# Optimization experiments

Measured on AMD Instinct MI355X. Metric: run time of the kernel, lower is better.

## Reference

```python
import jax, jax.numpy as jnp
import numpy as np

TEMP = 0.0005

def conv1d(x, w, b):
    # x: [B, Cin, T], w: [Cout, Cin, K] -> [B, Cout, T] with SAME padding
    out = jax.lax.conv_general_dilated(x, w, (1,), 'SAME', dimension_numbers=('NCH', 'OIH', 'NCH'))
    return out + b[None, :, None]

def setup_inputs() -> dict:
    key = jax.random.key(0)
    ks = jax.random.split(key, 24)
    B, Cs, T1 = 16, 80, 1000   # spec channels / mel frames
    Ct, T2 = 512, 200          # text channels / phonemes
    Ca, G = 80, 256            # attention channels / speaker embedding
    n = lambda i, shape: jax.random.normal(ks[i], shape, jnp.float32)
    w = lambda i, shape: n(i, shape) * 0.05
    return {
        'queries': n(0, (B, Cs, T1)),
        'keys': n(1, (B, Ct, T2)),
        'mask': jnp.ones((B, T2), jnp.int32),
        'attn_prior': jax.random.uniform(ks[2], (B, T1, T2), jnp.float32),
        'g': n(3, (B, G)),
        # key_proj: Conv(Ct -> 2Ct, k=3) -> ReLU -> Conv(2Ct -> Ca, k=1)
        'wk1': w(4, (2 * Ct, Ct, 3)), 'bk1': jnp.zeros((2 * Ct,), jnp.float32),
        'wk2': w(5, (Ca, 2 * Ct, 1)), 'bk2': jnp.zeros((Ca,), jnp.float32),
        # query_proj: Conv(Cs -> 2Cs, k=3) -> ReLU -> Conv(2Cs -> Cs, k=1) -> ReLU -> Conv(Cs -> Ca, k=1)
        'wq1': w(6, (2 * Cs, Cs, 3)), 'bq1': jnp.zeros((2 * Cs,), jnp.float32),
        'wq2': w(7, (Cs, 2 * Cs, 1)), 'bq2': jnp.zeros((Cs,), jnp.float32),
        'wq3': w(8, (Ca, Cs, 1)), 'bq3': jnp.zeros((Ca,), jnp.float32),
        # speaker projections (LinearNorm): gin -> n_text_channels / n_spec_channels
        'w_kspk': w(9, (Ct, G)), 'b_kspk': jnp.zeros((Ct,), jnp.float32),
        'w_qspk': w(10, (Cs, G)), 'b_qspk': jnp.zeros((Cs,), jnp.float32),
    }

def reference(queries, keys, mask, attn_prior, g, wk1, bk1, wk2, bk2, wq1, bq1, wq2, bq2, wq3, bq3, w_kspk, b_kspk, w_qspk, b_qspk):
    # speaker conditioning: same projected vector added at every time step
    keys = keys + (g @ w_kspk.T + b_kspk)[:, :, None]
    queries = queries + (g @ w_qspk.T + b_qspk)[:, :, None]
    # projections
    k_enc = conv1d(jax.nn.relu(conv1d(keys, wk1, bk1)), wk2, bk2)              # [B, Ca, T2]
    q = jax.nn.relu(conv1d(queries, wq1, bq1))
    q = jax.nn.relu(conv1d(q, wq2, bq2))
    q_enc = conv1d(q, wq3, bq3)                                                # [B, Ca, T1]
    # squared L2 distance via GEMM trick: |q|^2 + |k|^2 - 2 q.k  (same math as broadcast diff)
    q2 = jnp.sum(q_enc * q_enc, axis=1)[:, :, None]                            # [B, T1, 1]
    k2 = jnp.sum(k_enc * k_enc, axis=1)[:, None, :]                            # [B, 1, T2]
    qk = jnp.einsum('bct,bcs->bts', q_enc, k_enc)                              # [B, T1, T2]
    attn = (-TEMP * (q2 + k2 - 2.0 * qk))[:, None]                             # [B, 1, T1, T2]
    attn = jax.nn.log_softmax(attn, axis=3) + jnp.log(attn_prior[:, None] + 1e-8)
    attn_logprob = attn
    neg_inf = jnp.where(mask[:, None, None, :] == 0, -jnp.inf, 0.0)
    attn = jax.nn.softmax(attn + neg_inf, axis=3)
    return attn, attn_logprob
```

## Files before the change

### kernel.cpp

```cpp
#include <hip/hip_runtime.h>
#include <hip/hip_bf16.h>
#include <math.h>

#define NB 16
#define CS 80
#define T1 1000
#define CT 512
#define T2 200
#define CA 80
#define GD 256
#define C2T 1024
#define C2S 160
#define TEMP_F 0.0005f
#define ENC_STR 96

typedef __attribute__((ext_vector_type(8))) short short8;
typedef __attribute__((ext_vector_type(4))) float floatx4;

__device__ __forceinline__ short f2bf(float x) {
    unsigned u = __builtin_bit_cast(unsigned, x);
    unsigned r = (u + 0x7fffu + ((u >> 16) & 1u)) >> 16;
    return (short)r;
}

template <int COUT, int CIN, int KW, int COP, int CINP>
__device__ __forceinline__ void wpack_body(const float* __restrict__ w,
                                           short* __restrict__ wp, int bid) {
    constexpr int NC32 = CINP / 32;
    constexpr int NFRAG = (COP / 16) * KW * NC32;
    int gid = bid * 256 + threadIdx.x;
    int frag = gid >> 6, lane = gid & 63;
    if (frag >= NFRAG) return;
    int co16 = frag / (KW * NC32), rem = frag - co16 * (KW * NC32);
    int k = rem / NC32, ci32 = rem - k * NC32;
    int co = co16 * 16 + (lane & 15);
    int ci = ci32 * 32 + (lane >> 4) * 8;
    short8 v;
#pragma unroll
    for (int j = 0; j < 8; j++) {
        float f = 0.f;
        if (co < COUT && ci + j < CIN) f = w[((size_t)co * CIN + ci + j) * KW + k];
        v[j] = f2bf(f);
    }
    *(short8*)(wp + (size_t)frag * 512 + lane * 8) = v;
}

template <int C, int T>
__device__ __forceinline__ void addspkT_body(const float* __restrict__ in,
                                             const float* __restrict__ g,
                                             const float* __restrict__ w_spk,
                                             const float* __restrict__ b_spk,
                                             short* __restrict__ outT,
                                             float* sm, int bx, int by, int b) {
    float* spkS = sm;
    float* S = sm + 32;
    const int t0 = bx * 64, c0 = by * 32;
    const int tid = threadIdx.x;
    int cl = tid >> 3, part = tid & 7;
    int c = c0 + cl;
    float s = 0.f;
    if (c < C) {
        const float* wr = w_spk + (size_t)c * GD;
        const float* gr = g + b * GD;
        int j0 = part * 32;
#pragma unroll
        for (int j = 0; j < 32; j++) s += gr[j0 + j] * wr[j0 + j];
    }
    s += __shfl_xor(s, 1, 64); s += __shfl_xor(s, 2, 64); s += __shfl_xor(s, 4, 64);
    if (part == 0) spkS[cl] = s + ((c < C) ? b_spk[c] : 0.f);
    __syncthreads();
    for (int i = tid; i < 32 * 64; i += 256) {
        int cll = i >> 6, tl = i & 63;
        int gc = c0 + cll, gt = t0 + tl;
        float v = 0.f;
        if (gc < C && gt < T) v = in[((size_t)b * C + gc) * T + gt] + spkS[cll];
        S[cll * 65 + tl] = v;
    }
    __syncthreads();
    for (int i = tid; i < 64 * 32; i += 256) {
        int tl = i >> 5, cll = i & 31;
        int gt = t0 + tl, gc = c0 + cll;
        if (gc < C && gt < T) outT[((size_t)b * T + gt) * C + gc] = f2bf(S[cll * 65 + tl]);
    }
}

__global__ __launch_bounds__(256) void prep_kernel(
    const float* __restrict__ keys, const float* __restrict__ queries, const float* __restrict__ g,
    const float* __restrict__ wk1, const float* __restrict__ wq1, const float* __restrict__ wk2,
    const float* __restrict__ wq2, const float* __restrict__ wq3,
    const float* __restrict__ w_kspk, const float* __restrict__ b_kspk,
    const float* __restrict__ w_qspk, const float* __restrict__ b_qspk,
    short* __restrict__ wk1p, short* __restrict__ wq1p, short* __restrict__ wk2p,
    short* __restrict__ wq2p, short* __restrict__ wq3p,
    short* __restrict__ xkT, short* __restrict__ xqT) {
    __shared__ float sm[32 + 32 * 65];
    int bid = blockIdx.x;
    if (bid < 768) { wpack_body<C2T, CT, 3, C2T, CT>(wk1, wk1p, bid); return; }
    bid -= 768;
    if (bid < 27) { wpack_body<C2S, CS, 3, 192, 96>(wq1, wq1p, bid); return; }
    bid -= 27;
    if (bid < 40) { wpack_body<CA, C2T, 1, 80, 1024>(wk2, wk2p, bid); return; }
    bid -= 40;
    if (bid < 7) { wpack_body<CA, C2S, 1, 80, 160>(wq2, wq2p, bid); return; }
    bid -= 7;
    if (bid < 4) { wpack_body<CA, CS, 1, 80, 96>(wq3, wq3p, bid); return; }
    bid -= 4;
    if (bid < 1024) {
        int bx = bid & 3, by = (bid >> 2) & 15, b = bid >> 6;
        addspkT_body<CT, T2>(keys, g, w_kspk, b_kspk, xkT, sm, bx, by, b);
        return;
    }
    bid -= 1024;
    {
        int bx = bid & 15, by = (bid >> 4) % 3, b = bid / 48;
        addspkT_body<CS, T1>(queries, g, w_qspk, b_qspk, xqT, sm, bx, by, b);
    }
}

template <int CIN, int COUT, int T, int KW, bool RELU, int CICH, int NC32T>
__device__ __forceinline__ void conv_body(const short* __restrict__ xT,
                                          const short* __restrict__ wp,
                                          const float* __restrict__ bias,
                                          short* __restrict__ outT,
                                          short* Xs, int bx, int by, int b) {
    constexpr int TT = 128, COT = 64;
    constexpr int PAD = KW / 2;
    constexpr int XROWS = TT + KW - 1;
    constexpr int PITCH = CICH + 8;
    constexpr int NPC = CICH / 8;
    constexpr int NC32 = CICH / 32;
    constexpr int CINP = NC32T * 32;
    constexpr int NCHK = CINP / CICH;
    constexpr int NPIECE = XROWS * NPC;
    constexpr int NLD = (NPIECE + 255) / 256;

    const int t0 = bx * TT, co0 = by * COT;
    const int tid = threadIdx.x, wave = tid >> 6, lane = tid & 63;
    const int quad = lane >> 4, l16 = lane & 15;
    const int wt = wave * 32;
    const int co16_0 = co0 >> 4;
    const short* xb = xT + (size_t)b * T * CIN;

    floatx4 acc[4][2];
#pragma unroll
    for (int mi = 0; mi < 4; mi++)
#pragma unroll
        for (int ni = 0; ni < 2; ni++) acc[mi][ni] = (floatx4){0.f, 0.f, 0.f, 0.f};

    for (int i = tid; i < NPIECE; i += 256) {
        int r = i / NPC, p = i - r * NPC;
        int t = t0 + r - PAD, ci = p * 8;
        uint4 v = {0u, 0u, 0u, 0u};
        if ((unsigned)t < (unsigned)T && ci + 8 <= CIN)
            v = *(const uint4*)(xb + (size_t)t * CIN + ci);
        *(uint4*)(Xs + r * PITCH + p * 8) = v;
    }
    __syncthreads();

    for (int kc = 0; kc < NCHK; kc++) {
        uint4 tmp[NLD];
        if (NCHK > 1 && kc + 1 < NCHK) {
            int ci0n = (kc + 1) * CICH;
#pragma unroll
            for (int ld = 0; ld < NLD; ld++) {
                int i = tid + ld * 256;
                tmp[ld] = (uint4){0u, 0u, 0u, 0u};
                if (i < NPIECE) {
                    int r = i / NPC, p = i - r * NPC;
                    int t = t0 + r - PAD, ci = ci0n + p * 8;
                    if ((unsigned)t < (unsigned)T && ci + 8 <= CIN)
                        tmp[ld] = *(const uint4*)(xb + (size_t)t * CIN + ci);
                }
            }
        }
        const short* Xb = Xs + (NCHK > 1 ? (kc & 1) : 0) * XROWS * PITCH;
#pragma unroll
        for (int k = 0; k < KW; k++) {
#pragma unroll
            for (int kk = 0; kk < NC32; kk++) {
                int ci32 = kc * NC32 + kk;
                short8 a[4];
#pragma unroll
                for (int mi = 0; mi < 4; mi++)
                    a[mi] = *(const short8*)(wp +
                        ((size_t)((co16_0 + mi) * KW + k) * NC32T + ci32) * 512 + lane * 8);
#pragma unroll
                for (int ni = 0; ni < 2; ni++) {
                    short8 bb = *(const short8*)(Xb + (wt + ni * 16 + l16 + k) * PITCH +
                                                 kk * 32 + quad * 8);
#pragma unroll
                    for (int mi = 0; mi < 4; mi++)
                        acc[mi][ni] = __builtin_amdgcn_mfma_f32_16x16x32_bf16(a[mi], bb,
                                                                              acc[mi][ni], 0, 0, 0);
                }
            }
        }
        if (NCHK > 1 && kc + 1 < NCHK) {
            short* Xn = Xs + ((kc + 1) & 1) * XROWS * PITCH;
#pragma unroll
            for (int ld = 0; ld < NLD; ld++) {
                int i = tid + ld * 256;
                if (i < NPIECE) {
                    int r = i / NPC, p = i - r * NPC;
                    *(uint4*)(Xn + r * PITCH + p * 8) = tmp[ld];
                }
            }
            __syncthreads();
        }
    }
#pragma unroll
    for (int mi = 0; mi < 4; mi++) {
        int cb = co0 + mi * 16 + quad * 4;
        if (cb < COUT) {
            float4 bv = *(const float4*)(bias + cb);
#pragma unroll
            for (int ni = 0; ni < 2; ni++) {
                int t = t0 + wt + ni * 16 + l16;
                if (t < T) {
                    float v0 = acc[mi][ni][0] + bv.x, v1 = acc[mi][ni][1] + bv.y;
                    float v2 = acc[mi][ni][2] + bv.z, v3 = acc[mi][ni][3] + bv.w;
                    if (RELU) {
                        v0 = fmaxf(v0, 0.f); v1 = fmaxf(v1, 0.f);
                        v2 = fmaxf(v2, 0.f); v3 = fmaxf(v3, 0.f);
                    }
                    ushort4 o;
                    o.x = (unsigned short)f2bf(v0); o.y = (unsigned short)f2bf(v1);
                    o.z = (unsigned short)f2bf(v2); o.w = (unsigned short)f2bf(v3);
                    *(ushort4*)(outT + ((size_t)b * T + t) * COUT + cb) = o;
                }
            }
        }
    }
}

__global__ __launch_bounds__(256, 2) void conv_kernel(
    const short* __restrict__ xkT, const short* __restrict__ wk1p,
    const float* __restrict__ bk1, short* __restrict__ kh1T,
    const short* __restrict__ xqT, const short* __restrict__ wq1p,
    const float* __restrict__ bq1, short* __restrict__ qh1T) {
    __shared__ short sm[18720];
    int bid = blockIdx.x;
    if (bid < 512) {
        int bx = bid & 1, by = (bid >> 1) & 15, b = bid >> 5;
        conv_body<CT, C2T, T2, 3, true, 64, 16>(xkT, wk1p, bk1, kh1T, sm, bx, by, b);
    } else {
        int r = bid - 512;
        int bx = r & 7, by = (r >> 3) % 3, b = r / 24;
        conv_body<CS, C2S, T1, 3, true, 96, 3>(xqT, wq1p, bq1, qh1T, sm, bx, by, b);
    }
}

__device__ __forceinline__ void kgemm_body(const short* __restrict__ xT,
                                           const short* __restrict__ wp,
                                           const float* __restrict__ bias,
                                           short* __restrict__ outT,
                                           float* __restrict__ k2ws,
                                           short* sm, int bid) {
    constexpr int K = 1024, KCH = 128, PITCH = 136, NPC = 16, NCHK = 8;
    const int n0 = bid * 64;
    const int tid = threadIdx.x, wave = tid >> 6, lane = tid & 63;
    const int quad = lane >> 4, l16 = lane & 15;
    floatx4 acc[5];
#pragma unroll
    for (int mi = 0; mi < 5; mi++) acc[mi] = (floatx4){0.f, 0.f, 0.f, 0.f};

    for (int i = tid; i < 64 * NPC; i += 256) {
        int r = i / NPC, p = i - r * NPC;
        *(uint4*)(sm + r * PITCH + p * 8) = *(const uint4*)(xT + (size_t)(n0 + r) * K + p * 8);
    }
    __syncthreads();
    for (int kc = 0; kc < NCHK; kc++) {
        uint4 tmp[4];
        if (kc + 1 < NCHK) {
            int ci0 = (kc + 1) * KCH;
#pragma unroll
            for (int ld = 0; ld < 4; ld++) {
                int i = tid + ld * 256;
                int r = i / NPC, p = i - r * NPC;
                tmp[ld] = *(const uint4*)(xT + (size_t)(n0 + r) * K + ci0 + p * 8);
            }
        }
        const short* Xb = sm + (kc & 1) * 64 * PITCH;
#pragma unroll
        for (int kk = 0; kk < 4; kk++) {
            int ci32 = kc * 4 + kk;
            short8 bb = *(const short8*)(Xb + (wave * 16 + l16) * PITCH + kk * 32 + quad * 8);
#pragma unroll
            for (int mi = 0; mi < 5; mi++) {
                short8 a = *(const short8*)(wp + ((size_t)(mi * 32 + ci32)) * 512 + lane * 8);
                acc[mi] = __builtin_amdgcn_mfma_f32_16x16x32_bf16(a, bb, acc[mi], 0, 0, 0);
            }
        }
        if (kc + 1 < NCHK) {
            short* Xn = sm + ((kc + 1) & 1) * 64 * PITCH;
#pragma unroll
            for (int ld = 0; ld < 4; ld++) {
                int i = tid + ld * 256;
                int r = i / NPC, p = i - r * NPC;
                *(uint4*)(Xn + r * PITCH + p * 8) = tmp[ld];
            }
            __syncthreads();
        }
    }
    int n = n0 + wave * 16 + l16;
    float sq = 0.f;
#pragma unroll
    for (int mi = 0; mi < 5; mi++) {
        int cb = mi * 16 + quad * 4;
        float4 bv = *(const float4*)(bias + cb);
        float v0 = acc[mi][0] + bv.x, v1 = acc[mi][1] + bv.y;
        float v2 = acc[mi][2] + bv.z, v3 = acc[mi][3] + bv.w;
        sq += v0 * v0 + v1 * v1 + v2 * v2 + v3 * v3;
        ushort4 o;
        o.x = (unsigned short)f2bf(v0); o.y = (unsigned short)f2bf(v1);
        o.z = (unsigned short)f2bf(v2); o.w = (unsigned short)f2bf(v3);
        *(ushort4*)(outT + (size_t)n * ENC_STR + cb) = o;
    }
    if (quad < 2) *(uint4*)(outT + (size_t)n * ENC_STR + 80 + quad * 8) = (uint4){0u, 0u, 0u, 0u};
    sq += __shfl_xor(sq, 16, 64);
    sq += __shfl_xor(sq, 32, 64);
    if (quad == 0) k2ws[n] = sq;
}

__device__ __forceinline__ void qconv23_body(const short* __restrict__ h1,
                                             const short* __restrict__ w2p,
                                             const float* __restrict__ b2,
                                             const short* __restrict__ w3p,
                                             const float* __restrict__ b3,
                                             short* __restrict__ outT, short* sm, int bid) {
    constexpr int K1 = 160, P1 = 168, NPC1 = 20, P3 = 104;
    short* Xs = sm;
    short* Hs = sm + 64 * P1;
    const int n0 = bid * 64;
    const int tid = threadIdx.x, wave = tid >> 6, lane = tid & 63;
    const int quad = lane >> 4, l16 = lane & 15;

    for (int i = tid; i < 64 * NPC1; i += 256) {
        int r = i / NPC1, p = i - r * NPC1;
        *(uint4*)(Xs + r * P1 + p * 8) = *(const uint4*)(h1 + (size_t)(n0 + r) * K1 + p * 8);
    }
    if (tid < 128) *(uint4*)(Hs + (tid >> 1) * P3 + 80 + (tid & 1) * 8) = (uint4){0u, 0u, 0u, 0u};
    __syncthreads();

    floatx4 acc[5];
#pragma unroll
    for (int mi = 0; mi < 5; mi++) acc[mi] = (floatx4){0.f, 0.f, 0.f, 0.f};
#pragma unroll
    for (int kk = 0; kk < 5; kk++) {
        short8 bb = *(const short8*)(Xs + (wave * 16 + l16) * P1 + kk * 32 + quad * 8);
#pragma unroll
        for (int mi = 0; mi < 5; mi++) {
            short8 a = *(const short8*)(w2p + ((size_t)(mi * 5 + kk)) * 512 + lane * 8);
            acc[mi] = __builtin_amdgcn_mfma_f32_16x16x32_bf16(a, bb, acc[mi], 0, 0, 0);
        }
    }
#pragma unroll
    for (int mi = 0; mi < 5; mi++) {
        int cb = mi * 16 + quad * 4;
        float4 bv = *(const float4*)(b2 + cb);
        ushort4 o;
        o.x = (unsigned short)f2bf(fmaxf(acc[mi][0] + bv.x, 0.f));
        o.y = (unsigned short)f2bf(fmaxf(acc[mi][1] + bv.y, 0.f));
        o.z = (unsigned short)f2bf(fmaxf(acc[mi][2] + bv.z, 0.f));
        o.w = (unsigned short)f2bf(fmaxf(acc[mi][3] + bv.w, 0.f));
        *(ushort4*)(Hs + (wave * 16 + l16) * P3 + cb) = o;
    }
    __syncthreads();

    floatx4 acc3[5];
#pragma unroll
    for (int mi = 0; mi < 5; mi++) acc3[mi] = (floatx4){0.f, 0.f, 0.f, 0.f};
#pragma unroll
    for (int kk = 0; kk < 3; kk++) {
        short8 bb = *(const short8*)(Hs + (wave * 16 + l16) * P3 + kk * 32 + quad * 8);
#pragma unroll
        for (int mi = 0; mi < 5; mi++) {
            short8 a = *(const short8*)(w3p + ((size_t)(mi * 3 + kk)) * 512 + lane * 8);
            acc3[mi] = __builtin_amdgcn_mfma_f32_16x16x32_bf16(a, bb, acc3[mi], 0, 0, 0);
        }
    }
    int n = n0 + wave * 16 + l16;
#pragma unroll
    for (int mi = 0; mi < 5; mi++) {
        int cb = mi * 16 + quad * 4;
        float4 bv = *(const float4*)(b3 + cb);
        ushort4 o;
        o.x = (unsigned short)f2bf(acc3[mi][0] + bv.x);
        o.y = (unsigned short)f2bf(acc3[mi][1] + bv.y);
        o.z = (unsigned short)f2bf(acc3[mi][2] + bv.z);
        o.w = (unsigned short)f2bf(acc3[mi][3] + bv.w);
        *(ushort4*)(outT + (size_t)n * ENC_STR + cb) = o;
    }
    if (quad < 2) *(uint4*)(outT + (size_t)n * ENC_STR + 80 + quad * 8) = (uint4){0u, 0u, 0u, 0u};
}

__global__ __launch_bounds__(256, 2) void gemm_kernel(
    const short* __restrict__ kh1T, const short* __restrict__ wk2p,
    const float* __restrict__ bk2, short* __restrict__ k_encT, float* __restrict__ k2ws,
    const short* __restrict__ qh1T, const short* __restrict__ wq2p,
    const float* __restrict__ bq2, const short* __restrict__ wq3p,
    const float* __restrict__ bq3, short* __restrict__ q_encT) {
    __shared__ short sm[17408];
    int bid = blockIdx.x;
    if (bid < 50) kgemm_body(kh1T, wk2p, bk2, k_encT, k2ws, sm, bid);
    else qconv23_body(qh1T, wq2p, bq2, wq3p, bq3, q_encT, sm, bid - 50);
}

__device__ __forceinline__ float rmax16(float v) {
#pragma unroll
    for (int o = 1; o < 16; o <<= 1) v = fmaxf(v, __shfl_xor(v, o, 64));
    return v;
}
__device__ __forceinline__ float rsum16(float v) {
#pragma unroll
    for (int o = 1; o < 16; o <<= 1) v += __shfl_xor(v, o, 64);
    return v;
}

__global__ __launch_bounds__(256) void attn_kernel(const short* __restrict__ q_encT,
                                                   const short* __restrict__ k_encT,
                                                   const float* __restrict__ k2ws,
                                                   const float* __restrict__ prior,
                                                   const int* __restrict__ mask,
                                                   float* __restrict__ out_attn,
                                                   float* __restrict__ out_logp) {
    const int t10 = blockIdx.x * 64, b = blockIdx.y;
    const int tid = threadIdx.x, wave = tid >> 6, lane = tid & 63;
    const int quad = lane >> 4, l16 = lane & 15;

    float k2v[13]; int mskv[13];
#pragma unroll
    for (int n = 0; n < 13; n++) {
        int t2 = n * 16 + l16, t2c = t2 < T2 ? t2 : T2 - 1;
        k2v[n] = k2ws[b * T2 + t2c];
        mskv[n] = (t2 < T2) ? mask[b * T2 + t2] : 0;
    }
    const int t1base = t10 + wave * 16 + quad * 4;
    float pr[4][13];
#pragma unroll
    for (int r = 0; r < 4; r++) {
        int t1 = t1base + r, t1c = t1 < T1 ? t1 : T1 - 1;
#pragma unroll
        for (int n = 0; n < 13; n++) {
            int t2 = n * 16 + l16, t2c = t2 < T2 ? t2 : T2 - 1;
            pr[r][n] = prior[((size_t)b * T1 + t1c) * T2 + t2c];
        }
    }

    floatx4 acc[13];
#pragma unroll
    for (int n = 0; n < 13; n++) acc[n] = (floatx4){0.f, 0.f, 0.f, 0.f};
    const short* qb = q_encT + ((size_t)(b * T1 + t10 + wave * 16 + l16)) * ENC_STR + quad * 8;
    const short* kb = k_encT + ((size_t)(b * T2 + l16)) * ENC_STR + quad * 8;
#pragma unroll
    for (int kk = 0; kk < 3; kk++) {
        short8 a = *(const short8*)(qb + kk * 32);
#pragma unroll
        for (int n = 0; n < 13; n++) {
            short8 bb = *(const short8*)(kb + (size_t)n * 16 * ENC_STR + kk * 32);
            acc[n] = __builtin_amdgcn_mfma_f32_16x16x32_bf16(a, bb, acc[n], 0, 0, 0);
        }
    }

#pragma unroll
    for (int r = 0; r < 4; r++) {
        int t1 = t1base + r;
        bool t1ok = t1 < T1;
        float s[13], u[13];
        float mx = -INFINITY, mxu = -INFINITY;
#pragma unroll
        for (int n = 0; n < 13; n++) {
            int t2 = n * 16 + l16;
            float sv = (t2 < T2) ? TEMP_F * (2.f * acc[n][r] - k2v[n]) : -INFINITY;
            s[n] = sv;
            float uv = (t2 < T2) ? sv + __logf(pr[r][n] + 1e-8f) : -INFINITY;
            u[n] = uv;
            mx = fmaxf(mx, sv);
            mxu = fmaxf(mxu, (mskv[n] != 0) ? uv : -INFINITY);
        }
        float m = rmax16(mx);
        float m2 = rmax16(mxu);
        float se = 0.f, se2 = 0.f;
        float e2v[13];
#pragma unroll
        for (int n = 0; n < 13; n++) {
            se += (s[n] == -INFINITY) ? 0.f : __expf(s[n] - m);
            float e2 = (mskv[n] != 0) ? __expf(u[n] - m2) : 0.f;
            e2v[n] = e2;
            se2 += e2;
        }
        float logZ = __logf(rsum16(se));
        float invZ2 = 1.f / rsum16(se2);
        if (t1ok) {
#pragma unroll
            for (int n = 0; n < 13; n++) {
                int t2 = n * 16 + l16;
                if (t2 < T2) {
                    size_t o = ((size_t)b * T1 + t1) * T2 + t2;
                    out_attn[o] = e2v[n] * invZ2;
                    out_logp[o] = u[n] - m - logZ;
                }
            }
        }
    }
}

extern "C" void kernel_launch(void* const* d_in, const int* in_sizes, int n_in,
                              void* d_out, int out_size, void* d_ws, size_t ws_size,
                              hipStream_t stream) {
    const float* queries = (const float*)d_in[0];
    const float* keys    = (const float*)d_in[1];
    const int*   mask    = (const int*)d_in[2];
    const float* prior   = (const float*)d_in[3];
    const float* g       = (const float*)d_in[4];
    const float* wk1 = (const float*)d_in[5];
    const float* bk1 = (const float*)d_in[6];
    const float* wk2 = (const float*)d_in[7];
    const float* bk2 = (const float*)d_in[8];
    const float* wq1 = (const float*)d_in[9];
    const float* bq1 = (const float*)d_in[10];
    const float* wq2 = (const float*)d_in[11];
    const float* bq2 = (const float*)d_in[12];
    const float* wq3 = (const float*)d_in[13];
    const float* bq3 = (const float*)d_in[14];
    const float* w_kspk = (const float*)d_in[15];
    const float* b_kspk = (const float*)d_in[16];
    const float* w_qspk = (const float*)d_in[17];
    const float* b_qspk = (const float*)d_in[18];

    short* wsS   = (short*)d_ws;
    short* xkT   = wsS;
    short* xqT   = wsS + 1638400;
    short* wk1p  = wsS + 2918400;
    short* wq1p  = wsS + 4491264;
    short* wk2p  = wsS + 4546560;
    short* wq2p  = wsS + 4628480;
    short* wq3p  = wsS + 4641280;
    short* k_encT = wsS + 4648960;
    short* q_encT = wsS + 4957696;
    float* k2ws  = (float*)d_ws + 3248384;
    short* doS  = (short*)d_out;
    short* kh1T = doS;
    short* qh1T = doS + 3276800;

    prep_kernel<<<dim3(2638), dim3(256), 0, stream>>>(
        keys, queries, g, wk1, wq1, wk2, wq2, wq3,
        w_kspk, b_kspk, w_qspk, b_qspk,
        wk1p, wq1p, wk2p, wq2p, wq3p, xkT, xqT);
    conv_kernel<<<dim3(896), dim3(256), 0, stream>>>(xkT, wk1p, bk1, kh1T,
                                                     xqT, wq1p, bq1, qh1T);
    gemm_kernel<<<dim3(300), dim3(256), 0, stream>>>(kh1T, wk2p, bk2, k_encT, k2ws,
                                                     qh1T, wq2p, bq2, wq3p, bq3, q_encT);
    float* out_attn = (float*)d_out;
    float* out_logp = out_attn + (size_t)NB * T1 * T2;
    attn_kernel<<<dim3(16, NB), dim3(256), 0, stream>>>(q_encT, k_encT, k2ws, prior, mask,
                                                        out_attn, out_logp);
}
```

Before: 191.9 us.

## Fuse four stage kernels into one cooperative persistent kernel with grid syncs

Replaces the four separate launches (prep, conv, gemm, attn) with a single cooperative kernel of 512 persistent blocks that loops over virtual block indices and separates stages with grid-wide syncs. Shared-memory double buffering in the conv and gemm bodies becomes single buffering with an extra barrier, which cuts LDS use so two blocks can stay resident per CU. This aims to remove launch gaps and inter-kernel drain time. In exchange it loses prefetch overlap, pays grid-sync costs, and the attn and gemm stages use only part of the grid. A fallback to separate launches remains if the cooperative launch fails.

```diff
diff --git a/kernel.cpp b/kernel.cpp
--- a/kernel.cpp
+++ b/kernel.cpp
@@ -1,4 +1,5 @@
 #include <hip/hip_runtime.h>
+#include <hip/hip_cooperative_groups.h>
 #include <hip/hip_bf16.h>
 #include <math.h>
 
@@ -13,6 +14,7 @@
 #define C2S 160
 #define TEMP_F 0.0005f
 #define ENC_STR 96
+#define GRID 512
 
 typedef __attribute__((ext_vector_type(8))) short short8;
 typedef __attribute__((ext_vector_type(4))) float floatx4;
@@ -84,39 +86,6 @@
     }
 }
 
-__global__ __launch_bounds__(256) void prep_kernel(
-    const float* __restrict__ keys, const float* __restrict__ queries, const float* __restrict__ g,
-    const float* __restrict__ wk1, const float* __restrict__ wq1, const float* __restrict__ wk2,
-    const float* __restrict__ wq2, const float* __restrict__ wq3,
-    const float* __restrict__ w_kspk, const float* __restrict__ b_kspk,
-    const float* __restrict__ w_qspk, const float* __restrict__ b_qspk,
-    short* __restrict__ wk1p, short* __restrict__ wq1p, short* __restrict__ wk2p,
-    short* __restrict__ wq2p, short* __restrict__ wq3p,
-    short* __restrict__ xkT, short* __restrict__ xqT) {
-    __shared__ float sm[32 + 32 * 65];
-    int bid = blockIdx.x;
-    if (bid < 768) { wpack_body<C2T, CT, 3, C2T, CT>(wk1, wk1p, bid); return; }
-    bid -= 768;
-    if (bid < 27) { wpack_body<C2S, CS, 3, 192, 96>(wq1, wq1p, bid); return; }
-    bid -= 27;
-    if (bid < 40) { wpack_body<CA, C2T, 1, 80, 1024>(wk2, wk2p, bid); return; }
-    bid -= 40;
-    if (bid < 7) { wpack_body<CA, C2S, 1, 80, 160>(wq2, wq2p, bid); return; }
-    bid -= 7;
-    if (bid < 4) { wpack_body<CA, CS, 1, 80, 96>(wq3, wq3p, bid); return; }
-    bid -= 4;
-    if (bid < 1024) {
-        int bx = bid & 3, by = (bid >> 2) & 15, b = bid >> 6;
-        addspkT_body<CT, T2>(keys, g, w_kspk, b_kspk, xkT, sm, bx, by, b);
-        return;
-    }
-    bid -= 1024;
-    {
-        int bx = bid & 15, by = (bid >> 4) % 3, b = bid / 48;
-        addspkT_body<CS, T1>(queries, g, w_qspk, b_qspk, xqT, sm, bx, by, b);
-    }
-}
-
 template <int CIN, int COUT, int T, int KW, bool RELU, int CICH, int NC32T>
 __device__ __forceinline__ void conv_body(const short* __restrict__ xT,
                                           const short* __restrict__ wp,
@@ -148,12 +117,12 @@
         for (int ni = 0; ni < 2; ni++) acc[mi][ni] = (floatx4){0.f, 0.f, 0.f, 0.f};
 
     for (int i = tid; i < NPIECE; i += 256) {
-        int r = i / NPC, p = i - r * NPC;
-        int t = t0 + r - PAD, ci = p * 8;
+        int r = i / NPC, pp = i - r * NPC;
+        int t = t0 + r - PAD, ci = pp * 8;
         uint4 v = {0u, 0u, 0u, 0u};
         if ((unsigned)t < (unsigned)T && ci + 8 <= CIN)
             v = *(const uint4*)(xb + (size_t)t * CIN + ci);
-        *(uint4*)(Xs + r * PITCH + p * 8) = v;
+        *(uint4*)(Xs + r * PITCH + pp * 8) = v;
     }
     __syncthreads();
 
@@ -166,14 +135,13 @@
                 int i = tid + ld * 256;
                 tmp[ld] = (uint4){0u, 0u, 0u, 0u};
                 if (i < NPIECE) {
-                    int r = i / NPC, p = i - r * NPC;
-                    int t = t0 + r - PAD, ci = ci0n + p * 8;
+                    int r = i / NPC, pp = i - r * NPC;
+                    int t = t0 + r - PAD, ci = ci0n + pp * 8;
                     if ((unsigned)t < (unsigned)T && ci + 8 <= CIN)
                         tmp[ld] = *(const uint4*)(xb + (size_t)t * CIN + ci);
                 }
             }
         }
-        const short* Xb = Xs + (NCHK > 1 ? (kc & 1) : 0) * XROWS * PITCH;
 #pragma unroll
         for (int k = 0; k < KW; k++) {
 #pragma unroll
@@ -186,7 +154,7 @@
                         ((size_t)((co16_0 + mi) * KW + k) * NC32T + ci32) * 512 + lane * 8);
 #pragma unroll
                 for (int ni = 0; ni < 2; ni++) {
-                    short8 bb = *(const short8*)(Xb + (wt + ni * 16 + l16 + k) * PITCH +
+                    short8 bb = *(const short8*)(Xs + (wt + ni * 16 + l16 + k) * PITCH +
                                                  kk * 32 + quad * 8);
 #pragma unroll
                     for (int mi = 0; mi < 4; mi++)
@@ -196,13 +164,13 @@
             }
         }
         if (NCHK > 1 && kc + 1 < NCHK) {
-            short* Xn = Xs + ((kc + 1) & 1) * XROWS * PITCH;
+            __syncthreads();
 #pragma unroll
             for (int ld = 0; ld < NLD; ld++) {
                 int i = tid + ld * 256;
                 if (i < NPIECE) {
-                    int r = i / NPC, p = i - r * NPC;
-                    *(uint4*)(Xn + r * PITCH + p * 8) = tmp[ld];
+                    int r = i / NPC, pp = i - r * NPC;
+                    *(uint4*)(Xs + r * PITCH + pp * 8) = tmp[ld];
                 }
             }
             __syncthreads();
@@ -233,23 +201,6 @@
     }
 }
 
-__global__ __launch_bounds__(256, 2) void conv_kernel(
-    const short* __restrict__ xkT, const short* __restrict__ wk1p,
-    const float* __restrict__ bk1, short* __restrict__ kh1T,
-    const short* __restrict__ xqT, const short* __restrict__ wq1p,
-    const float* __restrict__ bq1, short* __restrict__ qh1T) {
-    __shared__ short sm[18720];
-    int bid = blockIdx.x;
-    if (bid < 512) {
-        int bx = bid & 1, by = (bid >> 1) & 15, b = bid >> 5;
-        conv_body<CT, C2T, T2, 3, true, 64, 16>(xkT, wk1p, bk1, kh1T, sm, bx, by, b);
-    } else {
-        int r = bid - 512;
-        int bx = r & 7, by = (r >> 3) % 3, b = r / 24;
-        conv_body<CS, C2S, T1, 3, true, 96, 3>(xqT, wq1p, bq1, qh1T, sm, bx, by, b);
-    }
-}
-
 __device__ __forceinline__ void kgemm_body(const short* __restrict__ xT,
                                            const short* __restrict__ wp,
                                            const float* __restrict__ bias,
@@ -265,8 +216,8 @@
     for (int mi = 0; mi < 5; mi++) acc[mi] = (floatx4){0.f, 0.f, 0.f, 0.f};
 
     for (int i = tid; i < 64 * NPC; i += 256) {
-        int r = i / NPC, p = i - r * NPC;
-        *(uint4*)(sm + r * PITCH + p * 8) = *(const uint4*)(xT + (size_t)(n0 + r) * K + p * 8);
+        int r = i / NPC, pp = i - r * NPC;
+        *(uint4*)(sm + r * PITCH + pp * 8) = *(const uint4*)(xT + (size_t)(n0 + r) * K + pp * 8);
     }
     __syncthreads();
     for (int kc = 0; kc < NCHK; kc++) {
@@ -276,15 +227,14 @@
 #pragma unroll
             for (int ld = 0; ld < 4; ld++) {
                 int i = tid + ld * 256;
-                int r = i / NPC, p = i - r * NPC;
-                tmp[ld] = *(const uint4*)(xT + (size_t)(n0 + r) * K + ci0 + p * 8);
-            }
-        }
-        const short* Xb = sm + (kc & 1) * 64 * PITCH;
+                int r = i / NPC, pp = i - r * NPC;
+                tmp[ld] = *(const uint4*)(xT + (size_t)(n0 + r) * K + ci0 + pp * 8);
+            }
+        }
 #pragma unroll
         for (int kk = 0; kk < 4; kk++) {
             int ci32 = kc * 4 + kk;
-            short8 bb = *(const short8*)(Xb + (wave * 16 + l16) * PITCH + kk * 32 + quad * 8);
+            short8 bb = *(const short8*)(sm + (wave * 16 + l16) * PITCH + kk * 32 + quad * 8);
 #pragma unroll
             for (int mi = 0; mi < 5; mi++) {
                 short8 a = *(const short8*)(wp + ((size_t)(mi * 32 + ci32)) * 512 + lane * 8);
@@ -292,12 +242,12 @@
             }
         }
         if (kc + 1 < NCHK) {
-            short* Xn = sm + ((kc + 1) & 1) * 64 * PITCH;
+            __syncthreads();
 #pragma unroll
             for (int ld = 0; ld < 4; ld++) {
                 int i = tid + ld * 256;
-                int r = i / NPC, p = i - r * NPC;
-                *(uint4*)(Xn + r * PITCH + p * 8) = tmp[ld];
+                int r = i / NPC, pp = i - r * NPC;
+                *(uint4*)(sm + r * PITCH + pp * 8) = tmp[ld];
             }
             __syncthreads();
         }
@@ -330,16 +280,15 @@
                                              short* __restrict__ outT, short* sm, int bid) {
     constexpr int K1 = 160, P1 = 168, NPC1 = 20, P3 = 104;
     short* Xs = sm;
-    short* Hs = sm + 64 * P1;
+    short* Hs = sm;
     const int n0 = bid * 64;
     const int tid = threadIdx.x, wave = tid >> 6, lane = tid & 63;
     const int quad = lane >> 4, l16 = lane & 15;
 
     for (int i = tid; i < 64 * NPC1; i += 256) {
-        int r = i / NPC1, p = i - r * NPC1;
-        *(uint4*)(Xs + r * P1 + p * 8) = *(const uint4*)(h1 + (size_t)(n0 + r) * K1 + p * 8);
-    }
-    if (tid < 128) *(uint4*)(Hs + (tid >> 1) * P3 + 80 + (tid & 1) * 8) = (uint4){0u, 0u, 0u, 0u};
+        int r = i / NPC1, pp = i - r * NPC1;
+        *(uint4*)(Xs + r * P1 + pp * 8) = *(const uint4*)(h1 + (size_t)(n0 + r) * K1 + pp * 8);
+    }
     __syncthreads();
 
     floatx4 acc[5];
@@ -354,6 +303,7 @@
             acc[mi] = __builtin_amdgcn_mfma_f32_16x16x32_bf16(a, bb, acc[mi], 0, 0, 0);
         }
     }
+    __syncthreads();
 #pragma unroll
     for (int mi = 0; mi < 5; mi++) {
         int cb = mi * 16 + quad * 4;
@@ -365,6 +315,7 @@
         o.w = (unsigned short)f2bf(fmaxf(acc[mi][3] + bv.w, 0.f));
         *(ushort4*)(Hs + (wave * 16 + l16) * P3 + cb) = o;
     }
+    if (quad < 3) *(uint4*)(Hs + (wave * 16 + l16) * P3 + 80 + quad * 8) = (uint4){0u, 0u, 0u, 0u};
     __syncthreads();
 
     floatx4 acc3[5];
@@ -394,18 +345,6 @@
     if (quad < 2) *(uint4*)(outT + (size_t)n * ENC_STR + 80 + quad * 8) = (uint4){0u, 0u, 0u, 0u};
 }
 
-__global__ __launch_bounds__(256, 2) void gemm_kernel(
-    const short* __restrict__ kh1T, const short* __restrict__ wk2p,
-    const float* __restrict__ bk2, short* __restrict__ k_encT, float* __restrict__ k2ws,
-    const short* __restrict__ qh1T, const short* __restrict__ wq2p,
-    const float* __restrict__ bq2, const short* __restrict__ wq3p,
-    const float* __restrict__ bq3, short* __restrict__ q_encT) {
-    __shared__ short sm[17408];
-    int bid = blockIdx.x;
-    if (bid < 50) kgemm_body(kh1T, wk2p, bk2, k_encT, k2ws, sm, bid);
-    else qconv23_body(qh1T, wq2p, bq2, wq3p, bq3, q_encT, sm, bid - 50);
-}
-
 __device__ __forceinline__ float rmax16(float v) {
 #pragma unroll
     for (int o = 1; o < 16; o <<= 1) v = fmaxf(v, __shfl_xor(v, o, 64));
@@ -417,14 +356,15 @@
     return v;
 }
 
-__global__ __launch_bounds__(256) void attn_kernel(const short* __restrict__ q_encT,
-                                                   const short* __restrict__ k_encT,
-                                                   const float* __restrict__ k2ws,
-                                                   const float* __restrict__ prior,
-                                                   const int* __restrict__ mask,
-                                                   float* __restrict__ out_attn,
-                                                   float* __restrict__ out_logp) {
-    const int t10 = blockIdx.x * 64, b = blockIdx.y;
+__device__ __forceinline__ void attn_body(int tix, int b,
+                                          const short* __restrict__ q_encT,
+                                          const short* __restrict__ k_encT,
+                                          const float* __restrict__ k2ws,
+                                          const float* __restrict__ prior,
+                                          const int* __restrict__ mask,
+                                          float* __restrict__ out_attn,
+                                          float* __restrict__ out_logp) {
+    const int t10 = tix * 64;
     const int tid = threadIdx.x, wave = tid >> 6, lane = tid & 63;
     const int quad = lane >> 4, l16 = lane & 15;
 
@@ -505,54 +445,141 @@
     }
 }
 
+struct KP {
+    const float* queries; const float* keys; const int* mask; const float* prior; const float* g;
+    const float* wk1; const float* bk1; const float* wk2; const float* bk2;
+    const float* wq1; const float* bq1; const float* wq2; const float* bq2;
+    const float* wq3; const float* bq3;
+    const float* w_kspk; const float* b_kspk; const float* w_qspk; const float* b_qspk;
+    short* wk1p; short* wq1p; short* wk2p; short* wq2p; short* wq3p;
+    short* xkT; short* xqT; short* k_encT; short* q_encT; float* k2ws;
+    short* kh1T; short* qh1T; float* out_attn; float* out_logp;
+};
+
+#define NPREP 2638
+#define NCONV 896
+
+__device__ __forceinline__ void prep_virt(int bid, const KP& p, float* smF) {
+    if (bid < 768) { wpack_body<C2T, CT, 3, C2T, CT>(p.wk1, p.wk1p, bid); return; }
+    bid -= 768;
+    if (bid < 27) { wpack_body<C2S, CS, 3, 192, 96>(p.wq1, p.wq1p, bid); return; }
+    bid -= 27;
+    if (bid < 40) { wpack_body<CA, C2T, 1, 80, 1024>(p.wk2, p.wk2p, bid); return; }
+    bid -= 40;
+    if (bid < 7) { wpack_body<CA, C2S, 1, 80, 160>(p.wq2, p.wq2p, bid); return; }
+    bid -= 7;
+    if (bid < 4) { wpack_body<CA, CS, 1, 80, 96>(p.wq3, p.wq3p, bid); return; }
+    bid -= 4;
+    if (bid < 1024) {
+        int bx = bid & 3, by = (bid >> 2) & 15, b = bid >> 6;
+        addspkT_body<CT, T2>(p.keys, p.g, p.w_kspk, p.b_kspk, p.xkT, smF, bx, by, b);
+        return;
+    }
+    bid -= 1024;
+    {
+        int bx = bid & 15, by = (bid >> 4) % 3, b = bid / 48;
+        addspkT_body<CS, T1>(p.queries, p.g, p.w_qspk, p.b_qspk, p.xqT, smF, bx, by, b);
+    }
+}
+
+__device__ __forceinline__ void conv_virt(int bid, const KP& p, short* sm) {
+    if (bid < 512) {
+        int bx = bid & 1, by = (bid >> 1) & 15, b = bid >> 5;
+        conv_body<CT, C2T, T2, 3, true, 64, 16>(p.xkT, p.wk1p, p.bk1, p.kh1T, sm, bx, by, b);
+    } else {
+        int r = bid - 512;
+        int bx = r & 7, by = (r >> 3) % 3, b = r / 24;
+        conv_body<CS, C2S, T1, 3, true, 96, 3>(p.xqT, p.wq1p, p.bq1, p.qh1T, sm, bx, by, b);
+    }
+}
+
+__global__ __launch_bounds__(256, 2) void fused_all(KP p) {
+    __shared__ __align__(16) short smS[13520];
+    cooperative_groups::grid_group gg = cooperative_groups::this_grid();
+
+    for (int vb = blockIdx.x; vb < NPREP; vb += GRID) {
+        __syncthreads();
+        prep_virt(vb, p, (float*)smS);
+    }
+    gg.sync();
+
+    for (int vb = blockIdx.x; vb < NCONV; vb += GRID) {
+        __syncthreads();
+        conv_virt(vb, p, smS);
+    }
+    gg.sync();
+
+    if (blockIdx.x < 50)
+        kgemm_body(p.kh1T, p.wk2p, p.bk2, p.k_encT, p.k2ws, smS, blockIdx.x);
+    else if (blockIdx.x < 300)
+        qconv23_body(p.qh1T, p.wq2p, p.bq2, p.wq3p, p.bq3, p.q_encT, smS, blockIdx.x - 50);
+    gg.sync();
+
+    if (blockIdx.x < 256)
+        attn_body(blockIdx.x & 15, blockIdx.x >> 4, p.q_encT, p.k_encT, p.k2ws,
+                  p.prior, p.mask, p.out_attn, p.out_logp);
+}
+
+__global__ __launch_bounds__(256) void prep_kernel_fb(KP p) {
+    __shared__ __align__(16) float smF[32 + 32 * 65];
+    prep_virt(blockIdx.x, p, smF);
+}
+__global__ __launch_bounds__(256, 2) void conv_kernel_fb(KP p) {
+    __shared__ __align__(16) short sm[13520];
+    conv_virt(blockIdx.x, p, sm);
+}
+__global__ __launch_bounds__(256, 2) void gemm_kernel_fb(KP p) {
+    __shared__ __align__(16) short sm[10752];
+    int bid = blockIdx.x;
+    if (bid < 50) kgemm_body(p.kh1T, p.wk2p, p.bk2, p.k_encT, p.k2ws, sm, bid);
+    else qconv23_body(p.qh1T, p.wq2p, p.bq2, p.wq3p, p.bq3, p.q_encT, sm, bid - 50);
+}
+__global__ __launch_bounds__(256) void attn_kernel_fb(KP p) {
+    attn_body(blockIdx.x, blockIdx.y, p.q_encT, p.k_encT, p.k2ws, p.prior, p.mask,
+              p.out_attn, p.out_logp);
+}
+
 extern "C" void kernel_launch(void* const* d_in, const int* in_sizes, int n_in,
                               void* d_out, int out_size, void* d_ws, size_t ws_size,
                               hipStream_t stream) {
-    const float* queries = (const float*)d_in[0];
-    const float* keys    = (const float*)d_in[1];
-    const int*   mask    = (const int*)d_in[2];
-    const float* prior   = (const float*)d_in[3];
-    const float* g       = (const float*)d_in[4];
-    const float* wk1 = (const float*)d_in[5];
-    const float* bk1 = (const float*)d_in[6];
-    const float* wk2 = (const float*)d_in[7];
-    const float* bk2 = (const float*)d_in[8];
-    const float* wq1 = (const float*)d_in[9];
-    const float* bq1 = (const float*)d_in[10];
-    const float* wq2 = (const float*)d_in[11];
-    const float* bq2 = (const float*)d_in[12];
-    const float* wq3 = (const float*)d_in[13];
-    const float* bq3 = (const float*)d_in[14];
-    const float* w_kspk = (const float*)d_in[15];
-    const float* b_kspk = (const float*)d_in[16];
-    const float* w_qspk = (const float*)d_in[17];
-    const float* b_qspk = (const float*)d_in[18];
-
-    short* wsS   = (short*)d_ws;
-    short* xkT   = wsS;
-    short* xqT   = wsS + 1638400;
-    short* wk1p  = wsS + 2918400;
-    short* wq1p  = wsS + 4491264;
-    short* wk2p  = wsS + 4546560;
-    short* wq2p  = wsS + 4628480;
-    short* wq3p  = wsS + 4641280;
-    short* k_encT = wsS + 4648960;
-    short* q_encT = wsS + 4957696;
-    float* k2ws  = (float*)d_ws + 3248384;
-    short* doS  = (short*)d_out;
-    short* kh1T = doS;
-    short* qh1T = doS + 3276800;
-
-    prep_kernel<<<dim3(2638), dim3(256), 0, stream>>>(
-        keys, queries, g, wk1, wq1, wk2, wq2, wq3,
-        w_kspk, b_kspk, w_qspk, b_qspk,
-        wk1p, wq1p, wk2p, wq2p, wq3p, xkT, xqT);
-    conv_kernel<<<dim3(896), dim3(256), 0, stream>>>(xkT, wk1p, bk1, kh1T,
-                                                     xqT, wq1p, bq1, qh1T);
-    gemm_kernel<<<dim3(300), dim3(256), 0, stream>>>(kh1T, wk2p, bk2, k_encT, k2ws,
-                                                     qh1T, wq2p, bq2, wq3p, bq3, q_encT);
-    float* out_attn = (float*)d_out;
-    float* out_logp = out_attn + (size_t)NB * T1 * T2;
-    attn_kernel<<<dim3(16, NB), dim3(256), 0, stream>>>(q_encT, k_encT, k2ws, prior, mask,
-                                                        out_attn, out_logp);
-}
+    KP p;
+    p.queries = (const float*)d_in[0];
+    p.keys    = (const float*)d_in[1];
+    p.mask    = (const int*)d_in[2];
+    p.prior   = (const float*)d_in[3];
+    p.g       = (const float*)d_in[4];
+    p.wk1 = (const float*)d_in[5];  p.bk1 = (const float*)d_in[6];
+    p.wk2 = (const float*)d_in[7];  p.bk2 = (const float*)d_in[8];
+    p.wq1 = (const float*)d_in[9];  p.bq1 = (const float*)d_in[10];
+    p.wq2 = (const float*)d_in[11]; p.bq2 = (const float*)d_in[12];
+    p.wq3 = (const float*)d_in[13]; p.bq3 = (const float*)d_in[14];
+    p.w_kspk = (const float*)d_in[15]; p.b_kspk = (const float*)d_in[16];
+    p.w_qspk = (const float*)d_in[17]; p.b_qspk = (const float*)d_in[18];
+
+    short* wsS = (short*)d_ws;
+    p.xkT   = wsS;
+    p.xqT   = wsS + 1638400;
+    p.wk1p  = wsS + 2918400;
+    p.wq1p  = wsS + 4491264;
+    p.wk2p  = wsS + 4546560;
+    p.wq2p  = wsS + 4628480;
+    p.wq3p  = wsS + 4641280;
+    p.k_encT = wsS + 4648960;
+    p.q_encT = wsS + 4957696;
+    p.k2ws  = (float*)d_ws + 3248384;
+    short* doS = (short*)d_out;
+    p.kh1T = doS;
+    p.qh1T = doS + 3276800;
+    p.out_attn = (float*)d_out;
+    p.out_logp = (float*)d_out + (size_t)NB * T1 * T2;
+
+    void* kargs[] = { (void*)&p };
+    hipError_t e = hipLaunchCooperativeKernel((const void*)fused_all, dim3(GRID), dim3(256),
+                                              kargs, 0, stream);
+    if (e != hipSuccess) {
+        prep_kernel_fb<<<dim3(NPREP), dim3(256), 0, stream>>>(p);
+        conv_kernel_fb<<<dim3(NCONV), dim3(256), 0, stream>>>(p);
+        gemm_kernel_fb<<<dim3(300), dim3(256), 0, stream>>>(p);
+        attn_kernel_fb<<<dim3(16, NB), dim3(256), 0, stream>>>(p);
+    }
+}
```

Result: slower. 419.5 us (+118.6%).
